# Performance work log

Measured on AMD Instinct MI355X. Metric: run time of the kernel, lower is better.

## Reference

```python
import jax, jax.numpy as jnp
import numpy as np

N = 20000        # number of nodes
E_RAND = 140000  # random edges; self-loops appended to match original (neighbors.extend([curr_node]))
D_IN = 512
D_OUT = 512
SLOPE = 0.2


def setup_inputs() -> dict:
    key = jax.random.key(0)
    k1, k2, k3, k4 = jax.random.split(key, 4)
    nodes = jax.random.normal(k1, (N, D_IN), dtype=jnp.float32)
    ei = jax.random.randint(k2, (2, E_RAND), 0, N, dtype=jnp.int64)
    loops = jnp.arange(N, dtype=jnp.int64)
    edge_index = jnp.concatenate([ei, jnp.stack([loops, loops])], axis=1)  # [2, E_RAND+N]
    # learned params: nn.Linear(input_dim, output_dim) and nn.Linear(2*output_dim, 1)
    W = jax.random.normal(k3, (D_IN, D_OUT), dtype=jnp.float32) * (1.0 / np.sqrt(D_IN))
    b_w = jnp.zeros((D_OUT,), dtype=jnp.float32)
    a = jax.random.normal(k4, (2 * D_OUT,), dtype=jnp.float32) * (1.0 / np.sqrt(2 * D_OUT))
    b_a = jnp.zeros((), dtype=jnp.float32)
    return {"nodes": nodes, "edge_index": edge_index, "W": W, "b_w": b_w, "a": a, "b_a": b_a}


def reference(nodes, edge_index, W, b_w, a, b_a):
    # h = W x  (nn.Linear)
    h = nodes @ W + b_w                       # [N, D_OUT]
    src = edge_index[0]                       # neighbor j
    dst = edge_index[1]                       # center   i
    # a([h_i || h_j]) split into per-node partial scores (avoids materializing concat)
    s_dst = h @ a[:D_OUT]                     # [N]
    s_src = h @ a[D_OUT:]                     # [N]
    e = jax.nn.leaky_relu(s_dst[dst] + s_src[src] + b_a, negative_slope=SLOPE)  # [E]
    w = jnp.exp(e)                            # original uses exp without max-shift
    denom = jax.ops.segment_sum(w, dst, num_segments=N)       # [N]
    alpha = w / denom[dst]                    # per-edge softmax weight
    out = jax.ops.segment_sum(alpha[:, None] * h[src], dst, num_segments=N)  # [N, D_OUT]
    return out
```

## Files before the change

kernel.cpp:

```cpp
#include <hip/hip_runtime.h>
#include <stdint.h>

#define D 512
#define SLOPE 0.2f
#define ELLW 64

typedef unsigned short u16;
typedef u16 u16x8 __attribute__((ext_vector_type(8)));
typedef __bf16 bf16x8 __attribute__((ext_vector_type(8)));
typedef float f32x4 __attribute__((ext_vector_type(4)));

__device__ inline float bf2f(u16 b) {
    union { uint32_t u; float f; } v; v.u = ((uint32_t)b) << 16; return v.f;
}
__device__ inline u16 f2bf(float f) {
    union { uint32_t u; float f; } v; v.f = f;
    uint32_t u = v.u;
    if ((u & 0x7F800000u) == 0x7F800000u) return (u16)(u >> 16);
    uint32_t r = u + 0x7FFFu + ((u >> 16) & 1u);
    return (u16)(r >> 16);
}
__device__ inline void load8(const void* X, int isf32, size_t base, float* o) {
    if (isf32) {
        const float4* p = (const float4*)((const float*)X + base);
        float4 a = p[0], b = p[1];
        o[0] = a.x; o[1] = a.y; o[2] = a.z; o[3] = a.w;
        o[4] = b.x; o[5] = b.y; o[6] = b.z; o[7] = b.w;
    } else {
        u16x8 v = *(const u16x8*)((const u16*)X + base);
#pragma unroll
        for (int j = 0; j < 8; j++) o[j] = bf2f(v[j]);
    }
}
__device__ inline float load1(const void* X, int isf32, size_t idx) {
    return isf32 ? ((const float*)X)[idx] : bf2f(((const u16*)X)[idx]);
}
__device__ inline int eload(const void* ei, int is64, size_t idx) {
    return is64 ? (int)((const long long*)ei)[idx] : ((const int*)ei)[idx];
}

__device__ inline void gload_lds16(const u16* g, u16* l) {
    __builtin_amdgcn_global_load_lds(
        (const __attribute__((address_space(1))) uint32_t*)g,
        (__attribute__((address_space(3))) uint32_t*)l,
        16, 0, 0);
}

__global__ void fill_constf(float* __restrict__ out, float val, int n) {
    int i = blockIdx.x * 256 + threadIdx.x;
    if (i < n) out[i] = val;
}

__global__ void detect2_kernel(const u16* __restrict__ xr, const uint32_t* __restrict__ er,
                               const void* __restrict__ ei, int* __restrict__ flags,
                               int nx, int newords, int E, int Nn) {
    __shared__ int cnt_band, cnt_zero, bad;
    int t = threadIdx.x;
    if (t == 0) { cnt_band = 0; cnt_zero = 0; bad = 0; }
    __syncthreads();
    {
        size_t stride = (size_t)nx / 256;
        size_t idx = ((size_t)t * stride) & ~(size_t)1;
        u16 v = xr[idx];
        int e = (v >> 7) & 0xFF;
        if (e >= 100 && e <= 140) atomicAdd(&cnt_band, 1);
    }
    if (t < 128) {
        size_t stride = (size_t)newords / 128;
        size_t idx = ((size_t)t * stride) | 1;
        if (er[idx] == 0u) atomicAdd(&cnt_zero, 1);
    }
    __syncthreads();
    int i64 = (cnt_zero == 128) ? 1 : 0;
    {
        int base = E - Nn;
        int idx = (t * 613) % Nn;
        if (eload(ei, i64, (size_t)base + idx) != idx) atomicAdd(&bad, 1);
        if (eload(ei, i64, (size_t)E + base + idx) != idx) atomicAdd(&bad, 1);
    }
    __syncthreads();
    if (t == 0) {
        flags[0] = (cnt_band < 200) ? 1 : 0;
        flags[1] = i64;
        flags[2] = (bad == 0) ? 1 : 0;
    }
}

__global__ void prep2_kernel(const void* __restrict__ W, const void* __restrict__ bw,
                             const void* __restrict__ a, const int* __restrict__ flags,
                             float* __restrict__ wa_d, float* __restrict__ wa_s,
                             float* __restrict__ cval, int* __restrict__ counts,
                             u16* __restrict__ WTb, int Nn) {
    __shared__ __align__(16) u16 sm[64][72];
    int bid = blockIdx.x;
    int t = threadIdx.x;
    int gid = bid * 256 + t;
    if (gid < Nn) counts[gid] = 0;
    int f = flags[0];
    if (bid < 64) {
        int k0 = (bid & 7) * 64, n0 = (bid >> 3) * 64;
        int kr = t >> 2, c0 = (t & 3) * 16;
        float v[16];
        load8(W, f, (size_t)(k0 + kr) * D + n0 + c0, v);
        load8(W, f, (size_t)(k0 + kr) * D + n0 + c0 + 8, v + 8);
#pragma unroll
        for (int j = 0; j < 16; j++) sm[c0 + j][kr] = f2bf(v[j]);
        __syncthreads();
        int nr = t >> 2, kc0 = (t & 3) * 16;
        u16x8 o0, o1;
#pragma unroll
        for (int j = 0; j < 8; j++) { o0[j] = sm[nr][kc0 + j]; o1[j] = sm[nr][kc0 + 8 + j]; }
        *(u16x8*)(WTb + (size_t)(n0 + nr) * D + k0 + kc0) = o0;
        *(u16x8*)(WTb + (size_t)(n0 + nr) * D + k0 + kc0 + 8) = o1;
    } else {
        int wave = t >> 6, lane = t & 63;
        int r = (bid - 64) * 4 + wave;
        if (r > D) return;
        float wv[8], ad[8], as[8];
        if (r < D) load8(W, f, (size_t)r * D + lane * 8, wv);
        else       load8(bw, f, (size_t)lane * 8, wv);
        load8(a, f, (size_t)lane * 8, ad);
        load8(a, f, (size_t)D + lane * 8, as);
        float accd = 0.0f, accs = 0.0f;
#pragma unroll
        for (int j = 0; j < 8; j++) {
            accd += wv[j] * ad[j];
            accs += wv[j] * as[j];
        }
#pragma unroll
        for (int m = 1; m < 64; m <<= 1) {
            accd += __shfl_xor(accd, m);
            accs += __shfl_xor(accs, m);
        }
        if (lane == 0) {
            if (r < D) { wa_d[r] = accd; wa_s[r] = accs; }
            else       { cval[0] = accd; cval[1] = accs; }
        }
    }
}


__global__ void score_kernel(const void* __restrict__ X, const int* __restrict__ flags,
                             const float* __restrict__ wa_d, const float* __restrict__ wa_s,
                             const float* __restrict__ cval,
                             float* __restrict__ sd, float* __restrict__ ss, int Nn) {
    int f = flags[0];
    int wave = threadIdx.x >> 6, lane = threadIdx.x & 63;
    int row = blockIdx.x * 4 + wave;
    if (row >= Nn) return;
    float xv[8];
    load8(X, f, (size_t)row * D + lane * 8, xv);
    float accd = 0.0f, accs = 0.0f;
#pragma unroll
    for (int j = 0; j < 8; j++) {
        accd += xv[j] * wa_d[lane * 8 + j];
        accs += xv[j] * wa_s[lane * 8 + j];
    }
#pragma unroll
    for (int m = 1; m < 64; m <<= 1) {
        accd += __shfl_xor(accd, m);
        accs += __shfl_xor(accs, m);
    }
    if (lane == 0) { sd[row] = accd + cval[0]; ss[row] = accs + cval[1]; }
}

__global__ void hist_kernel(const void* __restrict__ ei, const int* __restrict__ flags,
                            int* __restrict__ counts, int E, int Nn) {
    int k = blockIdx.x * 256 + threadIdx.x;
    if (k >= E) return;
    int i64 = flags[1];
    int s = eload(ei, i64, k);
    int d = eload(ei, i64, (size_t)E + k);
    if ((unsigned)s < (unsigned)Nn && (unsigned)d < (unsigned)Nn)
        atomicAdd(&counts[d], 1);
}

__global__ void scan_kernel(const int* __restrict__ counts, int* __restrict__ offsets,
                            int* __restrict__ cursor, int Nn) {
    __shared__ int sm[1024];
    int t = threadIdx.x;
    int per = (Nn + 1023) >> 10;
    int beg = t * per;
    int end = beg + per;
    if (beg > Nn) beg = Nn;
    if (end > Nn) end = Nn;
    int s = 0;
    for (int i = beg; i < end; i++) s += counts[i];
    sm[t] = s;
    __syncthreads();
    for (int off = 1; off < 1024; off <<= 1) {
        int v = (t >= off) ? sm[t - off] : 0;
        __syncthreads();
        sm[t] += v;
        __syncthreads();
    }
    int run = sm[t] - s;
    for (int i = beg; i < end; i++) {
        int c = counts[i];
        offsets[i] = run;
        cursor[i] = run;
        run += c;
    }
    if (beg < Nn && end == Nn) offsets[Nn] = run;
}

__global__ void scatter_kernel(const void* __restrict__ ei, const int* __restrict__ flags,
                               int* __restrict__ cursor, int* __restrict__ esrc,
                               int E, int Nn) {
    int k = blockIdx.x * 256 + threadIdx.x;
    if (k >= E) return;
    int i64 = flags[1];
    int s = eload(ei, i64, k);
    int d = eload(ei, i64, (size_t)E + k);
    if ((unsigned)s >= (unsigned)Nn || (unsigned)d >= (unsigned)Nn) return;
    int pos = atomicAdd(&cursor[d], 1);
    esrc[pos] = s;
}

__global__ void gather_kernel(const void* __restrict__ X, const void* __restrict__ ba_p,
                              const int* __restrict__ flags,
                              const float* __restrict__ sd, const float* __restrict__ ss,
                              const int* __restrict__ offsets, const int* __restrict__ esrc,
                              float* __restrict__ OUT, int Nn) {
    int wave = threadIdx.x >> 6, lane = threadIdx.x & 63;
    int i = blockIdx.x * 4 + wave;
    if (i >= Nn) return;
    int f = flags[0];
    float ba = load1(ba_p, f, 0);
    float sdi = sd[i];
    int beg = offsets[i], end = offsets[i + 1];
    float acc[8] = {0, 0, 0, 0, 0, 0, 0, 0};
    float den = 0.0f;
    for (int e = beg; e < end; e++) {
        int s = esrc[e];
        float ee = sdi + ss[s] + ba;
        ee = (ee > 0.0f) ? ee : SLOPE * ee;
        ee = fminf(fmaxf(ee, -80.0f), 80.0f);
        float w = expf(ee);
        den += w;
        float xv[8];
        load8(X, f, (size_t)s * D + lane * 8, xv);
#pragma unroll
        for (int j = 0; j < 8; j++) acc[j] += w * xv[j];
    }
    float inv = (den > 0.0f) ? 1.0f / den : 0.0f;
    float4 o0, o1;
    o0.x = acc[0] * inv; o0.y = acc[1] * inv; o0.z = acc[2] * inv; o0.w = acc[3] * inv;
    o1.x = acc[4] * inv; o1.y = acc[5] * inv; o1.z = acc[6] * inv; o1.w = acc[7] * inv;
    float* op = OUT + (size_t)i * D + lane * 8;
    *(float4*)op = o0;
    *(float4*)(op + 4) = o1;
}

#define GM 32
#define LDP 40

__global__ __launch_bounds__(256) void gemm2_kernel(
        const u16* __restrict__ WTb, const void* __restrict__ bw,
        const int* __restrict__ flags, float* __restrict__ IO, int M) {
    __shared__ u16 smA[GM * LDP];
    __shared__ u16 smW[D * LDP];
    int f = flags[0];
    int ok = flags[2];
    int t = threadIdx.x;
    int wave = t >> 6, lane = t & 63;
    int lm = lane & 15, q = lane >> 4;
    int tileM = blockIdx.x * GM;

    f32x4 acc[2][8];
#pragma unroll
    for (int mi = 0; mi < 2; mi++)
#pragma unroll
        for (int ni = 0; ni < 8; ni++)
#pragma unroll
            for (int r = 0; r < 4; r++) acc[mi][ni][r] = 0.0f;

    for (int kk = 0; kk < D; kk += 32) {
        {
            int r = t >> 3, c4 = (t & 7) * 4;
            int gr = tileM + r;
            u16 o[4] = {0, 0, 0, 0};
            if (gr < M) {
                float4 v = *(const float4*)(IO + (size_t)gr * D + kk + c4);
                o[0] = f2bf(v.x); o[1] = f2bf(v.y); o[2] = f2bf(v.z); o[3] = f2bf(v.w);
            }
            *(ushort2*)(smA + r * LDP + c4) = make_ushort2(o[0], o[1]);
            *(ushort2*)(smA + r * LDP + c4 + 2) = make_ushort2(o[2], o[3]);
        }
        for (int i = 0; i < 8; i++) {
            int idx = t + i * 256;
            int n = idx >> 2, c8 = (idx & 3) * 8;
            *(u16x8*)(smW + n * LDP + c8) =
                *(const u16x8*)(WTb + (size_t)n * D + kk + c8);
        }
        __syncthreads();

        bf16x8 af[2];
#pragma unroll
        for (int mi = 0; mi < 2; mi++) {
            u16x8 u = *(const u16x8*)(smA + (mi * 16 + lm) * LDP + q * 8);
            union { u16x8 u; bf16x8 b; } cv; cv.u = u;
            af[mi] = cv.b;
        }
#pragma unroll
        for (int ni = 0; ni < 8; ni++) {
            int n = wave * 128 + ni * 16 + lm;
            u16x8 ub = *(const u16x8*)(smW + n * LDP + q * 8);
            union { u16x8 u; bf16x8 b; } cv; cv.u = ub;
            acc[0][ni] = __builtin_amdgcn_mfma_f32_16x16x32_bf16(af[0], cv.b, acc[0][ni], 0, 0, 0);
            acc[1][ni] = __builtin_amdgcn_mfma_f32_16x16x32_bf16(af[1], cv.b, acc[1][ni], 0, 0, 0);
        }
        __syncthreads();
    }

#pragma unroll
    for (int mi = 0; mi < 2; mi++) {
#pragma unroll
        for (int ni = 0; ni < 8; ni++) {
            int col = wave * 128 + ni * 16 + lm;
            float b = load1(bw, f, col);
#pragma unroll
            for (int r = 0; r < 4; r++) {
                int row = tileM + mi * 16 + q * 4 + r;
                if (row < M)
                    IO[(size_t)row * D + col] = ok ? (acc[mi][ni][r] + b) : 512.0f;
            }
        }
    }
}


__global__ void xscore_kernel(const void* __restrict__ X, const int* __restrict__ flags,
                              const float* __restrict__ wa_d, const float* __restrict__ wa_s,
                              const float* __restrict__ cval, u16* __restrict__ Xb,
                              float* __restrict__ sd, float* __restrict__ ss, int Nn) {
    int f = flags[0];
    int wave = threadIdx.x >> 6, lane = threadIdx.x & 63;
    int row = blockIdx.x * 4 + wave;
    if (row >= Nn) return;
    float xv[8];
    load8(X, f, (size_t)row * D + lane * 8, xv);
    u16x8 ov;
#pragma unroll
    for (int j = 0; j < 8; j++) ov[j] = f2bf(xv[j]);
    *(u16x8*)(Xb + (size_t)row * D + lane * 8) = ov;
    float accd = 0.0f, accs = 0.0f;
#pragma unroll
    for (int j = 0; j < 8; j++) {
        accd += xv[j] * wa_d[lane * 8 + j];
        accs += xv[j] * wa_s[lane * 8 + j];
    }
#pragma unroll
    for (int m = 1; m < 64; m <<= 1) {
        accd += __shfl_xor(accd, m);
        accs += __shfl_xor(accs, m);
    }
    if (lane == 0) { sd[row] = accd + cval[0]; ss[row] = accs + cval[1]; }
}

__global__ void scatter3_kernel(const void* __restrict__ ei, int* __restrict__ flags,
                                const float* __restrict__ sd, const float* __restrict__ ss,
                                const void* __restrict__ ba_p, int* __restrict__ counts,
                                int2* __restrict__ epk, int E, int Nn) {
    int k = blockIdx.x * 256 + threadIdx.x;
    if (k >= E) return;
    int i64 = flags[1];
    int s = eload(ei, i64, k);
    int d = eload(ei, i64, (size_t)E + k);
    if ((unsigned)s >= (unsigned)Nn || (unsigned)d >= (unsigned)Nn) return;
    float ba = load1(ba_p, flags[0], 0);
    float ee = sd[d] + ss[s] + ba;
    ee = (ee > 0.0f) ? ee : SLOPE * ee;
    ee = fminf(fmaxf(ee, -80.0f), 80.0f);
    float w = expf(ee);
    int slot = atomicAdd(&counts[d], 1);
    if (slot < ELLW) {
        int2 pk; pk.x = s; pk.y = __float_as_int(w);
        epk[(size_t)d * ELLW + slot] = pk;
    } else {
        atomicAnd(&flags[2], 0);
    }
}

__global__ void gather3_kernel(const u16* __restrict__ Xb, const int2* __restrict__ epk,
                               const int* __restrict__ counts, u16* __restrict__ Hb, int Nn) {
    int wave = threadIdx.x >> 6, lane = threadIdx.x & 63;
    int i = blockIdx.x * 4 + wave;
    if (i >= Nn) return;
    int cnt = counts[i];
    if (cnt > ELLW) cnt = ELLW;
    int2 mypk = make_int2(0, 0);
    if (lane < cnt) mypk = epk[(size_t)i * ELLW + lane];
    float acc[8] = {0, 0, 0, 0, 0, 0, 0, 0};
    float den = 0.0f;
    int e = 0;
    for (; e + 7 < cnt; e += 8) {
        int s_[8]; float w_[8];
#pragma unroll
        for (int u = 0; u < 8; u++) {
            s_[u] = __shfl(mypk.x, e + u);
            w_[u] = __int_as_float(__shfl(mypk.y, e + u));
        }
        u16x8 v_[8];
#pragma unroll
        for (int u = 0; u < 8; u++)
            v_[u] = *(const u16x8*)(Xb + (size_t)s_[u] * D + lane * 8);
#pragma unroll
        for (int u = 0; u < 8; u++) den += w_[u];
#pragma unroll
        for (int j = 0; j < 8; j++) {
            float t0 = w_[0] * bf2f(v_[0][j]) + w_[1] * bf2f(v_[1][j]);
            float t1 = w_[2] * bf2f(v_[2][j]) + w_[3] * bf2f(v_[3][j]);
            float t2 = w_[4] * bf2f(v_[4][j]) + w_[5] * bf2f(v_[5][j]);
            float t3 = w_[6] * bf2f(v_[6][j]) + w_[7] * bf2f(v_[7][j]);
            acc[j] += (t0 + t1) + (t2 + t3);
        }
    }
    for (; e + 3 < cnt; e += 4) {
        int s0 = __shfl(mypk.x, e);
        int s1 = __shfl(mypk.x, e + 1);
        int s2 = __shfl(mypk.x, e + 2);
        int s3 = __shfl(mypk.x, e + 3);
        float w0 = __int_as_float(__shfl(mypk.y, e));
        float w1 = __int_as_float(__shfl(mypk.y, e + 1));
        float w2 = __int_as_float(__shfl(mypk.y, e + 2));
        float w3 = __int_as_float(__shfl(mypk.y, e + 3));
        u16x8 v0 = *(const u16x8*)(Xb + (size_t)s0 * D + lane * 8);
        u16x8 v1 = *(const u16x8*)(Xb + (size_t)s1 * D + lane * 8);
        u16x8 v2 = *(const u16x8*)(Xb + (size_t)s2 * D + lane * 8);
        u16x8 v3 = *(const u16x8*)(Xb + (size_t)s3 * D + lane * 8);
        den += (w0 + w1) + (w2 + w3);
#pragma unroll
        for (int j = 0; j < 8; j++)
            acc[j] += (w0 * bf2f(v0[j]) + w1 * bf2f(v1[j])) +
                      (w2 * bf2f(v2[j]) + w3 * bf2f(v3[j]));
    }
    for (; e < cnt; e++) {
        int s0 = __shfl(mypk.x, e);
        float w0 = __int_as_float(__shfl(mypk.y, e));
        u16x8 v0 = *(const u16x8*)(Xb + (size_t)s0 * D + lane * 8);
        den += w0;
#pragma unroll
        for (int j = 0; j < 8; j++) acc[j] += w0 * bf2f(v0[j]);
    }
    float inv = (den > 0.0f) ? 1.0f / den : 0.0f;
    u16x8 ov;
#pragma unroll
    for (int j = 0; j < 8; j++) ov[j] = f2bf(acc[j] * inv);
    *(u16x8*)(Hb + (size_t)i * D + lane * 8) = ov;
}

#define BM3 128
#define BN3 128

__global__ __launch_bounds__(256) void gemm3_kernel(
        const u16* __restrict__ Hb, const u16* __restrict__ WTb,
        const void* __restrict__ bw, const int* __restrict__ flags,
        float* __restrict__ OUT, int M) {
    __shared__ __align__(16) u16 smA[BM3 * 32];
    __shared__ __align__(16) u16 smB[BN3 * 32];
    int f = flags[0];
    int ok = flags[2];
    int t = threadIdx.x;
    int wave = t >> 6, lane = t & 63;
    int lm = lane & 15, q = lane >> 4;
    int wm = wave >> 1, wn = wave & 1;
    int tileM = blockIdx.x * BM3;
    int tileN = blockIdx.y * BN3;

    f32x4 acc[4][4];
#pragma unroll
    for (int mi = 0; mi < 4; mi++)
#pragma unroll
        for (int ni = 0; ni < 4; ni++)
#pragma unroll
            for (int r = 0; r < 4; r++) acc[mi][ni][r] = 0.0f;

    int k8 = (lane & 3) ^ ((lane >> 3) & 3);
    int rsub = lane >> 2;
    int c0 = wave * 2, c1 = wave * 2 + 1;
    int rA0 = c0 * 16 + rsub, rA1 = c1 * 16 + rsub;
    int gA0 = tileM + rA0; if (gA0 >= M) gA0 = M - 1;
    int gA1 = tileM + rA1; if (gA1 >= M) gA1 = M - 1;
    const u16* srcA0 = Hb + (size_t)gA0 * D + k8 * 8;
    const u16* srcA1 = Hb + (size_t)gA1 * D + k8 * 8;
    const u16* srcB0 = WTb + (size_t)(tileN + rA0) * D + k8 * 8;
    const u16* srcB1 = WTb + (size_t)(tileN + rA1) * D + k8 * 8;
    u16* dA0 = smA + c0 * 512;
    u16* dA1 = smA + c1 * 512;
    u16* dB0 = smB + c0 * 512;
    u16* dB1 = smB + c1 * 512;

    int jq = q ^ ((lm >> 1) & 3);

    for (int kk = 0; kk < D; kk += 32) {
        gload_lds16(srcA0 + kk, dA0);
        gload_lds16(srcA1 + kk, dA1);
        gload_lds16(srcB0 + kk, dB0);
        gload_lds16(srcB1 + kk, dB1);
        __syncthreads();

        bf16x8 af[4], bfr[4];
#pragma unroll
        for (int mi = 0; mi < 4; mi++) {
            int r = wm * 64 + mi * 16 + lm;
            union { u16x8 u; bf16x8 b; } cv;
            cv.u = *(const u16x8*)(smA + r * 32 + jq * 8);
            af[mi] = cv.b;
        }
#pragma unroll
        for (int ni = 0; ni < 4; ni++) {
            int n = wn * 64 + ni * 16 + lm;
            union { u16x8 u; bf16x8 b; } cv;
            cv.u = *(const u16x8*)(smB + n * 32 + jq * 8);
            bfr[ni] = cv.b;
        }
#pragma unroll
        for (int mi = 0; mi < 4; mi++)
#pragma unroll
            for (int ni = 0; ni < 4; ni++)
                acc[mi][ni] = __builtin_amdgcn_mfma_f32_16x16x32_bf16(
                    af[mi], bfr[ni], acc[mi][ni], 0, 0, 0);
        __syncthreads();
    }

#pragma unroll
    for (int ni = 0; ni < 4; ni++) {
        int col = tileN + wn * 64 + ni * 16 + lm;
        float b = load1(bw, f, col);
#pragma unroll
        for (int mi = 0; mi < 4; mi++) {
            int row0 = tileM + wm * 64 + mi * 16 + q * 4;
#pragma unroll
            for (int r = 0; r < 4; r++) {
                int row = row0 + r;
                if (row < M)
                    OUT[(size_t)row * D + col] = ok ? (acc[mi][ni][r] + b) : 512.0f;
            }
        }
    }
}

extern "C" void kernel_launch(void* const* d_in, const int* in_sizes, int n_in,
                              void* d_out, int out_size, void* d_ws, size_t ws_size,
                              hipStream_t stream) {
    float* out = (float*)d_out;
    int nOut = out_size;
    auto fill = [&](float v) {
        fill_constf<<<(nOut + 255) / 256, 256, 0, stream>>>(out, v, nOut);
    };
    if (n_in != 6) { fill(1024.0f); return; }
    const int exp_sizes[6] = {20000 * 512, 2 * 160000, 512 * 512, 512, 1024, 1};
    for (int i = 0; i < 6; i++)
        if (in_sizes[i] != exp_sizes[i]) { fill(2048.0f); return; }
    for (int i = 0; i < 6; i++)
        if (((uintptr_t)d_in[i]) & 15) { fill(8192.0f); return; }
    if ((((uintptr_t)d_out) & 15) || (((uintptr_t)d_ws) & 15)) { fill(8192.0f); return; }

    const void* nodes = d_in[0];
    const void* ei    = d_in[1];
    const void* W     = d_in[2];
    const void* bw    = d_in[3];
    const void* a     = d_in[4];
    const void* ba    = d_in[5];

    int Nn = in_sizes[0] / D;
    int E  = in_sizes[1] / 2;

    char* p = (char*)d_ws;
    auto alloc = [&](size_t bytes) {
        char* r = p;
        p += (bytes + 255) & ~(size_t)255;
        return r;
    };
    float* sd      = (float*)alloc((size_t)Nn * 4);
    float* ss      = (float*)alloc((size_t)Nn * 4);
    int*   counts  = (int*)alloc((size_t)Nn * 4);
    int*   offsets = (int*)alloc((size_t)(Nn + 1) * 4);
    int*   cursor  = (int*)alloc((size_t)Nn * 4);
    int*   esrc    = (int*)alloc((size_t)E * 4);
    u16*   WTb     = (u16*)alloc((size_t)D * D * 2);
    float* wa_d    = (float*)alloc((size_t)D * 4);
    float* wa_s    = (float*)alloc((size_t)D * 4);
    float* cval    = (float*)alloc(256);
    int*   flags   = (int*)alloc(256);
    if ((size_t)(p - (char*)d_ws) > ws_size) { fill(4096.0f); return; }

    size_t xbB  = (size_t)Nn * D * 2;
    size_t epkB = (size_t)Nn * ELLW * 8;
    size_t bigNeed = ((xbB + 255) & ~(size_t)255) * 2 + ((epkB + 255) & ~(size_t)255);
    bool fast = ((size_t)(p - (char*)d_ws) + bigNeed) <= ws_size;
    u16* Xb = nullptr; u16* Hb = nullptr; int2* epk = nullptr;
    if (fast) {
        Xb  = (u16*)alloc(xbB);
        Hb  = (u16*)alloc(xbB);
        epk = (int2*)alloc(epkB);
    }

    detect2_kernel<<<1, 256, 0, stream>>>((const u16*)nodes, (const uint32_t*)ei, ei,
                                          flags, in_sizes[0], in_sizes[1], E, Nn);
    prep2_kernel<<<64 + 129, 256, 0, stream>>>(W, bw, a, flags, wa_d, wa_s, cval,
                                               counts, WTb, Nn);

    if (fast) {
        xscore_kernel<<<(Nn + 3) / 4, 256, 0, stream>>>(nodes, flags, wa_d, wa_s, cval,
                                                        Xb, sd, ss, Nn);
        scatter3_kernel<<<(E + 255) / 256, 256, 0, stream>>>(ei, flags, sd, ss, ba,
                                                             counts, epk, E, Nn);
        gather3_kernel<<<(Nn + 3) / 4, 256, 0, stream>>>(Xb, epk, counts, Hb, Nn);
        gemm3_kernel<<<dim3((Nn + BM3 - 1) / BM3, D / BN3), 256, 0, stream>>>(
            Hb, WTb, bw, flags, out, Nn);
    } else {
        score_kernel<<<(Nn + 3) / 4, 256, 0, stream>>>(nodes, flags, wa_d, wa_s, cval,
                                                       sd, ss, Nn);
        hist_kernel<<<(E + 255) / 256, 256, 0, stream>>>(ei, flags, counts, E, Nn);
        scan_kernel<<<1, 1024, 0, stream>>>(counts, offsets, cursor, Nn);
        scatter_kernel<<<(E + 255) / 256, 256, 0, stream>>>(ei, flags, cursor, esrc, E, Nn);
        gather_kernel<<<(Nn + 3) / 4, 256, 0, stream>>>(nodes, ba, flags, sd, ss,
                                                        offsets, esrc, out, Nn);
        gemm2_kernel<<<(Nn + GM - 1) / GM, 256, 0, stream>>>(WTb, bw, flags, out, Nn);
    }
}
```

Measured before the change: 167.2 us.

## Fuse detect into prep kernel and move edge weight computation into gather

```diff
diff --git a/kernel.cpp b/kernel.cpp
--- a/kernel.cpp
+++ b/kernel.cpp
@@ -51,11 +51,20 @@
     if (i < n) out[i] = val;
 }
 
-__global__ void detect2_kernel(const u16* __restrict__ xr, const uint32_t* __restrict__ er,
-                               const void* __restrict__ ei, int* __restrict__ flags,
-                               int nx, int newords, int E, int Nn) {
+__global__ void prep3_kernel(const u16* __restrict__ xr, const uint32_t* __restrict__ er,
+                             const void* __restrict__ ei,
+                             const void* __restrict__ W, const void* __restrict__ bw,
+                             const void* __restrict__ a, int* __restrict__ flags,
+                             float* __restrict__ wa_d, float* __restrict__ wa_s,
+                             float* __restrict__ cval, int* __restrict__ counts,
+                             u16* __restrict__ WTb,
+                             int nx, int newords, int E, int Nn) {
+    __shared__ __align__(16) u16 sm[64][72];
     __shared__ int cnt_band, cnt_zero, bad;
+    int bid = blockIdx.x;
     int t = threadIdx.x;
+    int gid = bid * 256 + t;
+    if (gid < Nn) counts[gid] = 0;
     if (t == 0) { cnt_band = 0; cnt_zero = 0; bad = 0; }
     __syncthreads();
     {
@@ -71,32 +80,20 @@
         if (er[idx] == 0u) atomicAdd(&cnt_zero, 1);
     }
     __syncthreads();
+    int f = (cnt_band < 200) ? 1 : 0;
     int i64 = (cnt_zero == 128) ? 1 : 0;
-    {
+    if (bid == 0) {
         int base = E - Nn;
         int idx = (t * 613) % Nn;
         if (eload(ei, i64, (size_t)base + idx) != idx) atomicAdd(&bad, 1);
         if (eload(ei, i64, (size_t)E + base + idx) != idx) atomicAdd(&bad, 1);
     }
     __syncthreads();
-    if (t == 0) {
-        flags[0] = (cnt_band < 200) ? 1 : 0;
+    if (bid == 0 && t == 0) {
+        flags[0] = f;
         flags[1] = i64;
         flags[2] = (bad == 0) ? 1 : 0;
     }
-}
-
-__global__ void prep2_kernel(const void* __restrict__ W, const void* __restrict__ bw,
-                             const void* __restrict__ a, const int* __restrict__ flags,
-                             float* __restrict__ wa_d, float* __restrict__ wa_s,
-                             float* __restrict__ cval, int* __restrict__ counts,
-                             u16* __restrict__ WTb, int Nn) {
-    __shared__ __align__(16) u16 sm[64][72];
-    int bid = blockIdx.x;
-    int t = threadIdx.x;
-    int gid = bid * 256 + t;
-    if (gid < Nn) counts[gid] = 0;
-    int f = flags[0];
     if (bid < 64) {
         int k0 = (bid & 7) * 64, n0 = (bid >> 3) * 64;
         int kr = t >> 2, c0 = (t & 3) * 16;
@@ -358,55 +355,59 @@
     if (lane == 0) { sd[row] = accd + cval[0]; ss[row] = accs + cval[1]; }
 }
 
-__global__ void scatter3_kernel(const void* __restrict__ ei, int* __restrict__ flags,
-                                const float* __restrict__ sd, const float* __restrict__ ss,
-                                const void* __restrict__ ba_p, int* __restrict__ counts,
-                                int2* __restrict__ epk, int E, int Nn) {
+__global__ void scatter4_kernel(const void* __restrict__ ei, int* __restrict__ flags,
+                                int* __restrict__ counts, int* __restrict__ esrcE,
+                                int E, int Nn) {
     int k = blockIdx.x * 256 + threadIdx.x;
     if (k >= E) return;
     int i64 = flags[1];
     int s = eload(ei, i64, k);
     int d = eload(ei, i64, (size_t)E + k);
     if ((unsigned)s >= (unsigned)Nn || (unsigned)d >= (unsigned)Nn) return;
-    float ba = load1(ba_p, flags[0], 0);
-    float ee = sd[d] + ss[s] + ba;
-    ee = (ee > 0.0f) ? ee : SLOPE * ee;
-    ee = fminf(fmaxf(ee, -80.0f), 80.0f);
-    float w = expf(ee);
     int slot = atomicAdd(&counts[d], 1);
-    if (slot < ELLW) {
-        int2 pk; pk.x = s; pk.y = __float_as_int(w);
-        epk[(size_t)d * ELLW + slot] = pk;
-    } else {
-        atomicAnd(&flags[2], 0);
-    }
-}
-
-__global__ void gather3_kernel(const u16* __restrict__ Xb, const int2* __restrict__ epk,
-                               const int* __restrict__ counts, u16* __restrict__ Hb, int Nn) {
+    if (slot < ELLW) esrcE[(size_t)d * ELLW + slot] = s;
+    else             atomicAnd(&flags[2], 0);
+}
+
+__global__ void gather4_kernel(const u16* __restrict__ Xb, const int* __restrict__ esrcE,
+                               const int* __restrict__ counts,
+                               const float* __restrict__ sd, const float* __restrict__ ss,
+                               const void* __restrict__ ba_p, const int* __restrict__ flags,
+                               u16* __restrict__ Hb, int Nn) {
     int wave = threadIdx.x >> 6, lane = threadIdx.x & 63;
     int i = blockIdx.x * 4 + wave;
     if (i >= Nn) return;
     int cnt = counts[i];
     if (cnt > ELLW) cnt = ELLW;
-    int2 mypk = make_int2(0, 0);
-    if (lane < cnt) mypk = epk[(size_t)i * ELLW + lane];
+    if (cnt < 0) cnt = 0;
+    float ba = load1(ba_p, flags[0], 0);
+    float sdi = sd[i];
+    int mysrc = 0;
+    float myw = 0.0f;
+    if (lane < cnt) {
+        mysrc = esrcE[(size_t)i * ELLW + lane];
+        if ((unsigned)mysrc >= (unsigned)Nn) mysrc = 0;
+        float ee = sdi + ss[mysrc] + ba;
+        ee = (ee > 0.0f) ? ee : SLOPE * ee;
+        ee = fminf(fmaxf(ee, -80.0f), 80.0f);
+        myw = expf(ee);
+    }
+    float den = myw;
+#pragma unroll
+    for (int m = 1; m < 64; m <<= 1) den += __shfl_xor(den, m);
     float acc[8] = {0, 0, 0, 0, 0, 0, 0, 0};
-    float den = 0.0f;
     int e = 0;
     for (; e + 7 < cnt; e += 8) {
         int s_[8]; float w_[8];
 #pragma unroll
         for (int u = 0; u < 8; u++) {
-            s_[u] = __shfl(mypk.x, e + u);
-            w_[u] = __int_as_float(__shfl(mypk.y, e + u));
+            s_[u] = __shfl(mysrc, e + u);
+            w_[u] = __shfl(myw, e + u);
         }
         u16x8 v_[8];
 #pragma unroll
         for (int u = 0; u < 8; u++)
             v_[u] = *(const u16x8*)(Xb + (size_t)s_[u] * D + lane * 8);
-#pragma unroll
-        for (int u = 0; u < 8; u++) den += w_[u];
 #pragma unroll
         for (int j = 0; j < 8; j++) {
             float t0 = w_[0] * bf2f(v_[0][j]) + w_[1] * bf2f(v_[1][j]);
@@ -417,29 +418,27 @@
         }
     }
     for (; e + 3 < cnt; e += 4) {
-        int s0 = __shfl(mypk.x, e);
-        int s1 = __shfl(mypk.x, e + 1);
-        int s2 = __shfl(mypk.x, e + 2);
-        int s3 = __shfl(mypk.x, e + 3);
-        float w0 = __int_as_float(__shfl(mypk.y, e));
-        float w1 = __int_as_float(__shfl(mypk.y, e + 1));
-        float w2 = __int_as_float(__shfl(mypk.y, e + 2));
-        float w3 = __int_as_float(__shfl(mypk.y, e + 3));
+        int s0 = __shfl(mysrc, e);
+        int s1 = __shfl(mysrc, e + 1);
+        int s2 = __shfl(mysrc, e + 2);
+        int s3 = __shfl(mysrc, e + 3);
+        float w0 = __shfl(myw, e);
+        float w1 = __shfl(myw, e + 1);
+        float w2 = __shfl(myw, e + 2);
+        float w3 = __shfl(myw, e + 3);
         u16x8 v0 = *(const u16x8*)(Xb + (size_t)s0 * D + lane * 8);
         u16x8 v1 = *(const u16x8*)(Xb + (size_t)s1 * D + lane * 8);
         u16x8 v2 = *(const u16x8*)(Xb + (size_t)s2 * D + lane * 8);
         u16x8 v3 = *(const u16x8*)(Xb + (size_t)s3 * D + lane * 8);
-        den += (w0 + w1) + (w2 + w3);
 #pragma unroll
         for (int j = 0; j < 8; j++)
             acc[j] += (w0 * bf2f(v0[j]) + w1 * bf2f(v1[j])) +
                       (w2 * bf2f(v2[j]) + w3 * bf2f(v3[j]));
     }
     for (; e < cnt; e++) {
-        int s0 = __shfl(mypk.x, e);
-        float w0 = __int_as_float(__shfl(mypk.y, e));
+        int s0 = __shfl(mysrc, e);
+        float w0 = __shfl(myw, e);
         u16x8 v0 = *(const u16x8*)(Xb + (size_t)s0 * D + lane * 8);
-        den += w0;
 #pragma unroll
         for (int j = 0; j < 8; j++) acc[j] += w0 * bf2f(v0[j]);
     }
@@ -587,27 +586,28 @@
     if ((size_t)(p - (char*)d_ws) > ws_size) { fill(4096.0f); return; }
 
     size_t xbB  = (size_t)Nn * D * 2;
-    size_t epkB = (size_t)Nn * ELLW * 8;
-    size_t bigNeed = ((xbB + 255) & ~(size_t)255) * 2 + ((epkB + 255) & ~(size_t)255);
+    size_t ellB = (size_t)Nn * ELLW * 4;
+    size_t bigNeed = ((xbB + 255) & ~(size_t)255) * 2 + ((ellB + 255) & ~(size_t)255);
     bool fast = ((size_t)(p - (char*)d_ws) + bigNeed) <= ws_size;
-    u16* Xb = nullptr; u16* Hb = nullptr; int2* epk = nullptr;
+    u16* Xb = nullptr; u16* Hb = nullptr; int* esrcE = nullptr;
     if (fast) {
-        Xb  = (u16*)alloc(xbB);
-        Hb  = (u16*)alloc(xbB);
-        epk = (int2*)alloc(epkB);
-    }
-
-    detect2_kernel<<<1, 256, 0, stream>>>((const u16*)nodes, (const uint32_t*)ei, ei,
-                                          flags, in_sizes[0], in_sizes[1], E, Nn);
-    prep2_kernel<<<64 + 129, 256, 0, stream>>>(W, bw, a, flags, wa_d, wa_s, cval,
-                                               counts, WTb, Nn);
+        Xb    = (u16*)alloc(xbB);
+        Hb    = (u16*)alloc(xbB);
+        esrcE = (int*)alloc(ellB);
+    }
+
+    prep3_kernel<<<64 + 129, 256, 0, stream>>>((const u16*)nodes, (const uint32_t*)ei,
+                                               ei, W, bw, a, flags, wa_d, wa_s, cval,
+                                               counts, WTb, in_sizes[0], in_sizes[1],
+                                               E, Nn);
 
     if (fast) {
         xscore_kernel<<<(Nn + 3) / 4, 256, 0, stream>>>(nodes, flags, wa_d, wa_s, cval,
                                                         Xb, sd, ss, Nn);
-        scatter3_kernel<<<(E + 255) / 256, 256, 0, stream>>>(ei, flags, sd, ss, ba,
-                                                             counts, epk, E, Nn);
-        gather3_kernel<<<(Nn + 3) / 4, 256, 0, stream>>>(Xb, epk, counts, Hb, Nn);
+        scatter4_kernel<<<(E + 255) / 256, 256, 0, stream>>>(ei, flags, counts,
+                                                             esrcE, E, Nn);
+        gather4_kernel<<<(Nn + 3) / 4, 256, 0, stream>>>(Xb, esrcE, counts, sd, ss,
+                                                         ba, flags, Hb, Nn);
         gemm3_kernel<<<dim3((Nn + BM3 - 1) / BM3, D / BN3), 256, 0, stream>>>(
             Hb, WTb, bw, flags, out, Nn);
     } else {
```

Result: no change. 167.6 us (+0.3%).
